# Kernel tuning notes

Measured on AMD Instinct MI355X. Metric: run time of the kernel, lower is better.

## Reference

```python
import jax, jax.numpy as jnp
import numpy as np

B, V, H, W, T = 16, 8, 256, 256, 2000  # batch, max views, image HxW, diffusion steps
LINEAR_START, LINEAR_END = 1e-06, 0.01


def _gammas():
    # linear beta schedule -> cumulative product of alphas (float64 math, fp32 buffer)
    betas = np.linspace(LINEAR_START, LINEAR_END, T, dtype=np.float64)
    return jnp.asarray(np.cumprod(1.0 - betas), dtype=jnp.float32)


def setup_inputs() -> dict:
    key = jax.random.key(0)
    ks = jax.random.split(key, 9)
    return {
        "y_0": jax.random.normal(ks[0], (B, 3, H, W), jnp.float32),
        "y_cond": jax.random.normal(ks[1], (B, V, 3, H, W), jnp.float32),
        "angle": jax.random.uniform(ks[2], (B, 1), jnp.float32),
        "noise": jax.random.normal(ks[3], (B, 3, H, W), jnp.float32),
        "rand_u": jax.random.uniform(ks[4], (B, 1), jnp.float32),
        "Wk": jax.random.normal(ks[5], (4, 6), jnp.float32) * 0.1,  # 1x1-conv stub for denoise_fn
        "bk": jax.random.normal(ks[6], (4,), jnp.float32) * 0.1,
        "gammas": _gammas(),
        "view_count": jax.random.randint(ks[7], (B,), 1, V + 1, dtype=jnp.int32),
        "t": jax.random.randint(ks[8], (B,), 1, T, dtype=jnp.int32),
    }


def reference(y_0, y_cond, angle, noise, rand_u, Wk, bk, gammas, view_count, t):
    # extract(gammas, t-1) / extract(gammas, t) and interpolated sample gammas
    gamma_t1 = gammas[t - 1][:, None]                      # [B,1]
    gamma_t2 = gammas[t][:, None]                          # [B,1]
    sg = (gamma_t2 - gamma_t1) * rand_u + gamma_t1         # [B,1]
    # q_sample: y_noisy = sqrt(sg)*y_0 + sqrt(1-sg)*noise
    sg4 = sg[:, :, None, None]                             # [B,1,1,1]
    y_noisy = jnp.sqrt(sg4) * y_0 + jnp.sqrt(1.0 - sg4) * noise  # [B,3,H,W]

    # ragged view gather expressed densely: every (b, v<view_count[b]) view pairs
    # y_cond[b, v] with y_noisy[b] along channels -> [B,V,6,H,W]
    x = jnp.concatenate(
        [y_cond, jnp.broadcast_to(y_noisy[:, None], y_cond.shape)], axis=2
    )

    # denoise_fn stub: 1x1 conv + bias + (gamma + angle) additive modulation
    mod = (sg + angle)[:, 0]                               # [B]
    out = (jnp.einsum('oc,bvchw->bvohw', Wk, x)
           + bk[None, None, :, None, None]
           + 0.1 * mod[:, None, None, None, None])         # [B,V,4,H,W]

    noise_all = out[:, :, :3]                              # [B,V,3,H,W]
    logits = out[:, :, 3:]                                 # [B,V,1,H,W]

    # pad_sequence(padding_value=-inf) + softmax over the ragged view axis
    mask = jnp.arange(V)[None, :] < view_count[:, None]    # [B,V]
    logits = jnp.where(mask[:, :, None, None, None], logits, -jnp.inf)
    weights = jax.nn.softmax(logits, axis=1)               # padded views -> exactly 0

    noise_hat = jnp.sum(noise_all * weights, axis=1)       # [B,3,H,W]
    return jnp.mean((noise - noise_hat) ** 2)              # F.mse_loss default 'mean'
```

## Files before the change

kernel.cpp:

```cpp
#include <hip/hip_runtime.h>
#include <math.h>

#define BB   16
#define VV   8
#define HW_  65536
#define HWQ  16384
#define NQUAD (BB * HWQ)
#define NBLK 1024
#define NTHR 256
#define NPIX_D 3145728.0

#define F4(a, j) (((const float*)&(a))[j])

__global__ __launch_bounds__(NTHR) void pvs_main(
    const float* __restrict__ y0,
    const float* __restrict__ ycond,
    const float* __restrict__ angle,
    const float* __restrict__ noise,
    const float* __restrict__ rand_u,
    const float* __restrict__ Wk,
    const float* __restrict__ bk,
    const float* __restrict__ gammas,
    const int*   __restrict__ view_count,
    const int*   __restrict__ tt,
    float* __restrict__ partials)
{
    __shared__ float s_sq[BB], s_sq1[BB], s_mod[BB];
    __shared__ int   s_vc[BB];
    __shared__ float s_red[NTHR];

    if (threadIdx.x < BB) {
        int b = threadIdx.x;
        int t = tt[b];
        float g1 = gammas[t - 1];
        float g2 = gammas[t];
        float sg = (g2 - g1) * rand_u[b] + g1;
        s_sq[b]  = sqrtf(sg);
        s_sq1[b] = sqrtf(1.0f - sg);
        s_mod[b] = 0.1f * (sg + angle[b]);
        s_vc[b]  = view_count[b];
    }
    __syncthreads();

    float wk[4][6], bkr[4];
    #pragma unroll
    for (int o = 0; o < 4; ++o) {
        bkr[o] = bk[o];
        #pragma unroll
        for (int c = 0; c < 6; ++c) wk[o][c] = Wk[o * 6 + c];
    }

    float acc = 0.0f;
    for (int q = blockIdx.x * NTHR + threadIdx.x; q < NQUAD; q += NBLK * NTHR) {
        int blk = q >> 8;
        int b   = blk & (BB - 1);
        int hw  = ((((blk >> 4) << 8) | (q & 255)) << 2);
        float sq = s_sq[b], sq1 = s_sq1[b], md = s_mod[b];
        const int vcs = __builtin_amdgcn_readfirstlane(s_vc[b]);

        float4 y0v[3], nzv[3];
        #pragma unroll
        for (int c = 0; c < 3; ++c) {
            y0v[c] = *(const float4*)(y0    + (b * 3 + c) * HW_ + hw);
            nzv[c] = *(const float4*)(noise + (b * 3 + c) * HW_ + hw);
        }
        float4 ycv[VV][3];
        #pragma unroll
        for (int v = 0; v < VV; ++v) {
            if (v < vcs) {
                #pragma unroll
                for (int c = 0; c < 3; ++c) {
                    ycv[v][c] = *(const float4*)(ycond + ((b * VV + v) * 3 + c) * HW_ + hw);
                }
            } else {
                #pragma unroll
                for (int c = 0; c < 3; ++c) {
                    ycv[v][c] = make_float4(0.f, 0.f, 0.f, 0.f);
                }
            }
        }

        #pragma unroll
        for (int j = 0; j < 4; ++j) {
            float yn0 = fmaf(sq, F4(y0v[0], j), sq1 * F4(nzv[0], j));
            float yn1 = fmaf(sq, F4(y0v[1], j), sq1 * F4(nzv[1], j));
            float yn2 = fmaf(sq, F4(y0v[2], j), sq1 * F4(nzv[2], j));

            float base[4];
            #pragma unroll
            for (int o = 0; o < 4; ++o) {
                base[o] = fmaf(wk[o][3], yn0,
                          fmaf(wk[o][4], yn1,
                          fmaf(wk[o][5], yn2, bkr[o] + md)));
            }

            float S = 0.0f, sx0 = 0.0f, sx1 = 0.0f, sx2 = 0.0f;
            #pragma unroll
            for (int v = 0; v < VV; ++v) {
                if (v < vcs) {
                    float x0 = F4(ycv[v][0], j);
                    float x1 = F4(ycv[v][1], j);
                    float x2 = F4(ycv[v][2], j);
                    float o3 = fmaf(wk[3][0], x0,
                               fmaf(wk[3][1], x1,
                               fmaf(wk[3][2], x2, base[3])));
                    float w  = __expf(o3);
                    S   += w;
                    sx0  = fmaf(w, x0, sx0);
                    sx1  = fmaf(w, x1, sx1);
                    sx2  = fmaf(w, x2, sx2);
                }
            }
            float nh0 = fmaf(wk[0][0], sx0,
                        fmaf(wk[0][1], sx1,
                        fmaf(wk[0][2], sx2, base[0] * S)));
            float nh1 = fmaf(wk[1][0], sx0,
                        fmaf(wk[1][1], sx1,
                        fmaf(wk[1][2], sx2, base[1] * S)));
            float nh2 = fmaf(wk[2][0], sx0,
                        fmaf(wk[2][1], sx1,
                        fmaf(wk[2][2], sx2, base[2] * S)));
            float invS = 1.0f / S;
            float d0 = F4(nzv[0], j) - nh0 * invS;
            float d1 = F4(nzv[1], j) - nh1 * invS;
            float d2 = F4(nzv[2], j) - nh2 * invS;
            acc = fmaf(d0, d0, fmaf(d1, d1, fmaf(d2, d2, acc)));
        }
    }

    s_red[threadIdx.x] = acc;
    __syncthreads();
    #pragma unroll
    for (int s = NTHR / 2; s > 0; s >>= 1) {
        if (threadIdx.x < s) s_red[threadIdx.x] += s_red[threadIdx.x + s];
        __syncthreads();
    }
    if (threadIdx.x == 0) partials[blockIdx.x] = s_red[0];
}

__global__ __launch_bounds__(256) void pvs_reduce(const float* __restrict__ partials,
                                                 float* __restrict__ out)
{
    __shared__ double s[256];
    double a = 0.0;
    for (int i = threadIdx.x; i < NBLK; i += 256) a += (double)partials[i];
    s[threadIdx.x] = a;
    __syncthreads();
    #pragma unroll
    for (int st = 128; st > 0; st >>= 1) {
        if (threadIdx.x < st) s[threadIdx.x] += s[threadIdx.x + st];
        __syncthreads();
    }
    if (threadIdx.x == 0) out[0] = (float)(s[0] / NPIX_D);
}

extern "C" void kernel_launch(void* const* d_in, const int* in_sizes, int n_in,
                              void* d_out, int out_size, void* d_ws, size_t ws_size,
                              hipStream_t stream) {
    const float* y0      = (const float*)d_in[0];
    const float* ycond   = (const float*)d_in[1];
    const float* angle   = (const float*)d_in[2];
    const float* noise   = (const float*)d_in[3];
    const float* rand_u  = (const float*)d_in[4];
    const float* Wk      = (const float*)d_in[5];
    const float* bk      = (const float*)d_in[6];
    const float* gammas  = (const float*)d_in[7];
    const int*   vcp     = (const int*)d_in[8];
    const int*   tt      = (const int*)d_in[9];

    float* partials = (float*)d_ws;
    float* out      = (float*)d_out;

    pvs_main<<<NBLK, NTHR, 0, stream>>>(y0, ycond, angle, noise, rand_u,
                                        Wk, bk, gammas, vcp, tt, partials);
    pvs_reduce<<<1, 256, 0, stream>>>(partials, out);
}
```

Before: 23.77 us.

## Use one-wave blocks, one quad per thread, with shuffle reduction

Replaces the grid-stride loop of 1024x256-thread blocks with 4096 single-wavefront blocks, each handling 256 pixels of one batch element and one float4 quad per thread. Per-batch scalars are computed per block directly rather than via shared memory plus a barrier, and the block reduction becomes a wave shuffle instead of a shared-memory tree with many syncthreads. This removes barriers and LDS traffic and may raise occupancy, but it launches more small blocks and makes the final reduce sum 4096 partials.

```diff
diff --git a/kernel.cpp b/kernel.cpp
--- a/kernel.cpp
+++ b/kernel.cpp
@@ -4,10 +4,8 @@
 #define BB   16
 #define VV   8
 #define HW_  65536
-#define HWQ  16384
-#define NQUAD (BB * HWQ)
-#define NBLK 1024
-#define NTHR 256
+#define NBLK 4096
+#define NTHR 64
 #define NPIX_D 3145728.0
 
 #define F4(a, j) (((const float*)&(a))[j])
@@ -25,22 +23,19 @@
     const int*   __restrict__ tt,
     float* __restrict__ partials)
 {
-    __shared__ float s_sq[BB], s_sq1[BB], s_mod[BB];
-    __shared__ int   s_vc[BB];
-    __shared__ float s_red[NTHR];
+    const int tid = threadIdx.x;
+    const int b   = blockIdx.x & (BB - 1);
+    const int pos = blockIdx.x >> 4;
+    const int hw  = (pos << 8) | (tid << 2);
 
-    if (threadIdx.x < BB) {
-        int b = threadIdx.x;
-        int t = tt[b];
-        float g1 = gammas[t - 1];
-        float g2 = gammas[t];
-        float sg = (g2 - g1) * rand_u[b] + g1;
-        s_sq[b]  = sqrtf(sg);
-        s_sq1[b] = sqrtf(1.0f - sg);
-        s_mod[b] = 0.1f * (sg + angle[b]);
-        s_vc[b]  = view_count[b];
-    }
-    __syncthreads();
+    const int   t  = tt[b];
+    const float g1 = gammas[t - 1];
+    const float g2 = gammas[t];
+    const float sg = (g2 - g1) * rand_u[b] + g1;
+    const float sq  = sqrtf(sg);
+    const float sq1 = sqrtf(1.0f - sg);
+    const float md  = 0.1f * (sg + angle[b]);
+    const int vcs = __builtin_amdgcn_readfirstlane(view_count[b]);
 
     float wk[4][6], bkr[4];
     #pragma unroll
@@ -50,92 +45,79 @@
         for (int c = 0; c < 6; ++c) wk[o][c] = Wk[o * 6 + c];
     }
 
+    float4 y0v[3], nzv[3];
+    #pragma unroll
+    for (int c = 0; c < 3; ++c) {
+        y0v[c] = *(const float4*)(y0    + (b * 3 + c) * HW_ + hw);
+        nzv[c] = *(const float4*)(noise + (b * 3 + c) * HW_ + hw);
+    }
+    float4 ycv[VV][3];
+    #pragma unroll
+    for (int v = 0; v < VV; ++v) {
+        if (v < vcs) {
+            #pragma unroll
+            for (int c = 0; c < 3; ++c) {
+                ycv[v][c] = *(const float4*)(ycond + ((b * VV + v) * 3 + c) * HW_ + hw);
+            }
+        } else {
+            #pragma unroll
+            for (int c = 0; c < 3; ++c) {
+                ycv[v][c] = make_float4(0.f, 0.f, 0.f, 0.f);
+            }
+        }
+    }
+
     float acc = 0.0f;
-    for (int q = blockIdx.x * NTHR + threadIdx.x; q < NQUAD; q += NBLK * NTHR) {
-        int blk = q >> 8;
-        int b   = blk & (BB - 1);
-        int hw  = ((((blk >> 4) << 8) | (q & 255)) << 2);
-        float sq = s_sq[b], sq1 = s_sq1[b], md = s_mod[b];
-        const int vcs = __builtin_amdgcn_readfirstlane(s_vc[b]);
+    #pragma unroll
+    for (int j = 0; j < 4; ++j) {
+        float yn0 = fmaf(sq, F4(y0v[0], j), sq1 * F4(nzv[0], j));
+        float yn1 = fmaf(sq, F4(y0v[1], j), sq1 * F4(nzv[1], j));
+        float yn2 = fmaf(sq, F4(y0v[2], j), sq1 * F4(nzv[2], j));
 
-        float4 y0v[3], nzv[3];
+        float base[4];
         #pragma unroll
-        for (int c = 0; c < 3; ++c) {
-            y0v[c] = *(const float4*)(y0    + (b * 3 + c) * HW_ + hw);
-            nzv[c] = *(const float4*)(noise + (b * 3 + c) * HW_ + hw);
+        for (int o = 0; o < 4; ++o) {
+            base[o] = fmaf(wk[o][3], yn0,
+                      fmaf(wk[o][4], yn1,
+                      fmaf(wk[o][5], yn2, bkr[o] + md)));
         }
-        float4 ycv[VV][3];
+
+        float S = 0.0f, sx0 = 0.0f, sx1 = 0.0f, sx2 = 0.0f;
         #pragma unroll
         for (int v = 0; v < VV; ++v) {
             if (v < vcs) {
-                #pragma unroll
-                for (int c = 0; c < 3; ++c) {
-                    ycv[v][c] = *(const float4*)(ycond + ((b * VV + v) * 3 + c) * HW_ + hw);
-                }
-            } else {
-                #pragma unroll
-                for (int c = 0; c < 3; ++c) {
-                    ycv[v][c] = make_float4(0.f, 0.f, 0.f, 0.f);
-                }
+                float x0 = F4(ycv[v][0], j);
+                float x1 = F4(ycv[v][1], j);
+                float x2 = F4(ycv[v][2], j);
+                float o3 = fmaf(wk[3][0], x0,
+                           fmaf(wk[3][1], x1,
+                           fmaf(wk[3][2], x2, base[3])));
+                float w  = __expf(o3);
+                S   += w;
+                sx0  = fmaf(w, x0, sx0);
+                sx1  = fmaf(w, x1, sx1);
+                sx2  = fmaf(w, x2, sx2);
             }
         }
-
-        #pragma unroll
-        for (int j = 0; j < 4; ++j) {
-            float yn0 = fmaf(sq, F4(y0v[0], j), sq1 * F4(nzv[0], j));
-            float yn1 = fmaf(sq, F4(y0v[1], j), sq1 * F4(nzv[1], j));
-            float yn2 = fmaf(sq, F4(y0v[2], j), sq1 * F4(nzv[2], j));
-
-            float base[4];
-            #pragma unroll
-            for (int o = 0; o < 4; ++o) {
-                base[o] = fmaf(wk[o][3], yn0,
-                          fmaf(wk[o][4], yn1,
-                          fmaf(wk[o][5], yn2, bkr[o] + md)));
-            }
-
-            float S = 0.0f, sx0 = 0.0f, sx1 = 0.0f, sx2 = 0.0f;
-            #pragma unroll
-            for (int v = 0; v < VV; ++v) {
-                if (v < vcs) {
-                    float x0 = F4(ycv[v][0], j);
-                    float x1 = F4(ycv[v][1], j);
-                    float x2 = F4(ycv[v][2], j);
-                    float o3 = fmaf(wk[3][0], x0,
-                               fmaf(wk[3][1], x1,
-                               fmaf(wk[3][2], x2, base[3])));
-                    float w  = __expf(o3);
-                    S   += w;
-                    sx0  = fmaf(w, x0, sx0);
-                    sx1  = fmaf(w, x1, sx1);
-                    sx2  = fmaf(w, x2, sx2);
-                }
-            }
-            float nh0 = fmaf(wk[0][0], sx0,
-                        fmaf(wk[0][1], sx1,
-                        fmaf(wk[0][2], sx2, base[0] * S)));
-            float nh1 = fmaf(wk[1][0], sx0,
-                        fmaf(wk[1][1], sx1,
-                        fmaf(wk[1][2], sx2, base[1] * S)));
-            float nh2 = fmaf(wk[2][0], sx0,
-                        fmaf(wk[2][1], sx1,
-                        fmaf(wk[2][2], sx2, base[2] * S)));
-            float invS = 1.0f / S;
-            float d0 = F4(nzv[0], j) - nh0 * invS;
-            float d1 = F4(nzv[1], j) - nh1 * invS;
-            float d2 = F4(nzv[2], j) - nh2 * invS;
-            acc = fmaf(d0, d0, fmaf(d1, d1, fmaf(d2, d2, acc)));
-        }
+        float nh0 = fmaf(wk[0][0], sx0,
+                    fmaf(wk[0][1], sx1,
+                    fmaf(wk[0][2], sx2, base[0] * S)));
+        float nh1 = fmaf(wk[1][0], sx0,
+                    fmaf(wk[1][1], sx1,
+                    fmaf(wk[1][2], sx2, base[1] * S)));
+        float nh2 = fmaf(wk[2][0], sx0,
+                    fmaf(wk[2][1], sx1,
+                    fmaf(wk[2][2], sx2, base[2] * S)));
+        float invS = 1.0f / S;
+        float d0 = F4(nzv[0], j) - nh0 * invS;
+        float d1 = F4(nzv[1], j) - nh1 * invS;
+        float d2 = F4(nzv[2], j) - nh2 * invS;
+        acc = fmaf(d0, d0, fmaf(d1, d1, fmaf(d2, d2, acc)));
     }
 
-    s_red[threadIdx.x] = acc;
-    __syncthreads();
     #pragma unroll
-    for (int s = NTHR / 2; s > 0; s >>= 1) {
-        if (threadIdx.x < s) s_red[threadIdx.x] += s_red[threadIdx.x + s];
-        __syncthreads();
-    }
-    if (threadIdx.x == 0) partials[blockIdx.x] = s_red[0];
+    for (int s = 32; s > 0; s >>= 1) acc += __shfl_down(acc, s, 64);
+    if (tid == 0) partials[blockIdx.x] = acc;
 }
 
 __global__ __launch_bounds__(256) void pvs_reduce(const float* __restrict__ partials,
```

Result: slower. 26.52 us (+11.5%).
